# Performance work log

Hardware: AMD Instinct MI355X
Metric: run time of the kernel (lower is better)

## Reference

```python
import jax, jax.numpy as jnp
import numpy as np

# Dimensions
N, C_IN, C_OUT, T, V = 64, 64, 64, 256, 25   # batch, channels, frames, joints
K, G = 3, 8                                   # num_subset, groups


def batch_norm(x, gamma, beta, eps=1e-5):
    # BatchNorm2d in training mode: biased batch stats over (N, T, V) per channel.
    mean = jnp.mean(x, axis=(0, 2, 3), keepdims=True)
    var = jnp.var(x, axis=(0, 2, 3), keepdims=True)
    g = gamma.reshape(1, -1, 1, 1)
    b = beta.reshape(1, -1, 1, 1)
    return g * (x - mean) * jax.lax.rsqrt(var + eps) + b


def setup_inputs() -> dict:
    key = jax.random.key(0)
    k0, k1, k2 = jax.random.split(key, 3)
    x0 = jax.random.normal(k0, (N, C_IN, T, V), dtype=jnp.float32)
    # decoupled adjacency parameter [num_subset, groups, V, V] (non-negative, adjacency-like)
    decoupled_A = jax.random.uniform(k1, (K, G, V, V), dtype=jnp.float32)
    scale = float(np.sqrt(0.5 / (C_OUT * K)))
    linear_weight = jax.random.normal(k2, (C_IN, C_OUT * K), dtype=jnp.float32) * scale
    linear_bias = jnp.full((1, C_OUT * K, 1, 1), 1e-6, dtype=jnp.float32)
    bn0_gamma = jnp.ones((C_OUT * K,), dtype=jnp.float32)
    bn0_beta = jnp.zeros((C_OUT * K,), dtype=jnp.float32)
    bn_gamma = jnp.ones((C_OUT,), dtype=jnp.float32)
    bn_beta = jnp.zeros((C_OUT,), dtype=jnp.float32)
    return {
        "x0": x0,
        "decoupled_A": decoupled_A,
        "linear_weight": linear_weight,
        "linear_bias": linear_bias,
        "bn0_gamma": bn0_gamma,
        "bn0_beta": bn0_beta,
        "bn_gamma": bn_gamma,
        "bn_beta": bn_beta,
    }


def reference(x0, decoupled_A, linear_weight, linear_bias,
              bn0_gamma, bn0_beta, bn_gamma, bn_beta):
    # Expand grouped adjacency to per-output-channel: [K, C_OUT, V, V]
    learn_adj = jnp.tile(decoupled_A, (1, C_OUT // G, 1, 1))
    # Degree normalization: A @ diag(1/(colsum+1e-3)) == divide columns by column sums.
    deg = jnp.sum(learn_adj, axis=2, keepdims=True)          # [K, C_OUT, 1, V]
    normed_adj = learn_adj / (deg + 0.001)                    # [K, C_OUT, V, V]

    # Pointwise channel mix: [N, C_IN, T, V] -> [N, K*C_OUT, T, V]
    x = jnp.einsum('nctw,cd->ndtw', x0, linear_weight) + linear_bias
    x = batch_norm(x, bn0_gamma, bn0_beta)

    n, kc, t, v = x.shape
    x = x.reshape(n, K, kc // K, t, v)                        # [N, K, C_OUT, T, V]
    # Per-channel graph propagation summed over subsets.
    x = jnp.einsum('nkctv,kcvw->nctw', x, normed_adj)         # [N, C_OUT, T, V]
    x = batch_norm(x, bn_gamma, bn_beta)

    x = x + x0  # identity residual (in_channels == out_channels)
    return jax.nn.relu(x)
```

## Files before the change

### kernel.cpp

```cpp
#include <hip/hip_runtime.h>
#include <hip/hip_bf16.h>

#define N_    64
#define CIN   64
#define COUT  64
#define T_    256
#define V_    25
#define K_    3
#define G_    8
#define D_    192
#define TV    6400
#define P_    409600.0f
#define NBLK1 1600

typedef __attribute__((ext_vector_type(8))) short bf16x8;
typedef __attribute__((ext_vector_type(4))) float f32x4;

__device__ __forceinline__ float bf2f(unsigned short u) {
    unsigned int x = ((unsigned int)u) << 16;
    return __uint_as_float(x);
}
__device__ __forceinline__ unsigned short f2bf(float f) {
    unsigned int x = __float_as_uint(f);
    unsigned int lsb = (x >> 16) & 1u;
    x += 0x7fffu + lsb;
    return (unsigned short)(x >> 16);
}

__global__ __launch_bounds__(256, 4) void k1_mfma(const float* __restrict__ x0,
                                                  const float* __restrict__ W,
                                                  const float* __restrict__ bias,
                                                  unsigned short* __restrict__ z,
                                                  float* __restrict__ part) {
    __shared__ unsigned short zb[4][16 * 68];
    __shared__ float ps[4][12][16], pq[4][12][16];
    int p0  = blockIdx.x * 256;
    int n   = p0 / TV;
    int tvb = p0 % TV;
    int wv  = threadIdx.x >> 6;
    int l   = threadIdx.x & 63;
    int l15 = l & 15;
    int kg  = l >> 4;
    int wbase = tvb + wv * 64;
    const float* xn = x0 + (size_t)n * CIN * TV;

    bf16x8 afr[4][2];
#pragma unroll
    for (int m = 0; m < 4; ++m)
#pragma unroll
        for (int kk = 0; kk < 2; ++kk)
#pragma unroll
            for (int j = 0; j < 8; ++j) {
                int c = kk * 32 + kg * 8 + j;
                afr[m][kk][j] = (short)f2bf(xn[(size_t)c * TV + wbase + m * 16 + l15]);
            }

    unsigned short* zn = z + (size_t)n * D_ * TV;
    unsigned short* zw = &zb[wv][0];
#pragma unroll 1
    for (int dt = 0; dt < 12; ++dt) {
        int dcol = dt * 16 + l15;
        bf16x8 bfr[2];
#pragma unroll
        for (int kk = 0; kk < 2; ++kk)
#pragma unroll
            for (int j = 0; j < 8; ++j) {
                int c = kk * 32 + kg * 8 + j;
                bfr[kk][j] = (short)f2bf(W[c * D_ + dcol]);
            }
        float bv = bias[dcol];
        f32x4 acc[4];
#pragma unroll
        for (int m = 0; m < 4; ++m) {
            acc[m][0] = bv; acc[m][1] = bv; acc[m][2] = bv; acc[m][3] = bv;
        }
#pragma unroll
        for (int m = 0; m < 4; ++m) {
            acc[m] = __builtin_amdgcn_mfma_f32_16x16x32_bf16(afr[m][0], bfr[0], acc[m], 0, 0, 0);
            acc[m] = __builtin_amdgcn_mfma_f32_16x16x32_bf16(afr[m][1], bfr[1], acc[m], 0, 0, 0);
        }
        float s = 0.f, sq = 0.f;
#pragma unroll
        for (int m = 0; m < 4; ++m)
#pragma unroll
            for (int r = 0; r < 4; ++r) {
                float v = acc[m][r];
                s += v; sq += v * v;
            }
        s  += __shfl_xor(s, 16, 64);  s  += __shfl_xor(s, 32, 64);
        sq += __shfl_xor(sq, 16, 64); sq += __shfl_xor(sq, 32, 64);
        if (kg == 0) { ps[wv][dt][l15] = s; pq[wv][dt][l15] = sq; }
#pragma unroll
        for (int m = 0; m < 4; ++m) {
            uint2 pk;
            pk.x = (unsigned int)f2bf(acc[m][0]) | ((unsigned int)f2bf(acc[m][1]) << 16);
            pk.y = (unsigned int)f2bf(acc[m][2]) | ((unsigned int)f2bf(acc[m][3]) << 16);
            *(uint2*)(&zw[l15 * 68 + m * 16 + kg * 4]) = pk;
        }
#pragma unroll
        for (int i = 0; i < 4; ++i) {
            int dR  = i * 4 + kg;
            int tvo = l15 * 4;
            uint2 v = *(const uint2*)(&zw[dR * 68 + tvo]);
            *(uint2*)(zn + (size_t)(dt * 16 + dR) * TV + wbase + tvo) = v;
        }
    }
    __syncthreads();
    int tid = threadIdx.x;
    if (tid < D_) {
        int dt = tid >> 4, lo = tid & 15;
        float s = ps[0][dt][lo] + ps[1][dt][lo] + ps[2][dt][lo] + ps[3][dt][lo];
        float q = pq[0][dt][lo] + pq[1][dt][lo] + pq[2][dt][lo] + pq[3][dt][lo];
        part[(size_t)blockIdx.x * 384 + tid]        = s;
        part[(size_t)blockIdx.x * 384 + 192 + tid]  = q;
    }
}

__global__ __launch_bounds__(64) void k1c_reduce(const float* __restrict__ part,
                                                 float* __restrict__ sum0,
                                                 float* __restrict__ sumsq0) {
    int idx = blockIdx.x;
    int l = threadIdx.x;
    float s = 0.f;
    for (int b = l; b < NBLK1; b += 64) s += part[(size_t)b * 384 + idx];
#pragma unroll
    for (int off = 32; off > 0; off >>= 1) s += __shfl_down(s, off, 64);
    if (l == 0) {
        if (idx < D_) sum0[idx] = s;
        else          sumsq0[idx - D_] = s;
    }
}

__global__ __launch_bounds__(256, 1) void k2_prep(const float* __restrict__ A,
                                                  const float* __restrict__ g0,
                                                  const float* __restrict__ b0,
                                                  const float* __restrict__ sum0,
                                                  const float* __restrict__ sumsq0,
                                                  float* a, float* b,
                                                  float* nadj, float* bconst) {
    int tid = threadIdx.x;
    if (tid < D_) {
        float m   = sum0[tid] / P_;
        float var = sumsq0[tid] / P_ - m * m;
        float sc  = g0[tid] * rsqrtf(var + 1e-5f);
        a[tid] = sc;
        b[tid] = b0[tid] - sc * m;
    }
    for (int idx = tid; idx < K_ * G_ * V_; idx += 256) {
        int w  = idx % V_;
        int kg = idx / V_;
        const float* Ap = A + kg * V_ * V_;
        float cs = 0.f;
        for (int v = 0; v < V_; ++v) cs += Ap[v * V_ + w];
        float inv = 1.f / (cs + 1e-3f);
        for (int v = 0; v < V_; ++v) nadj[kg * V_ * V_ + v * V_ + w] = Ap[v * V_ + w] * inv;
    }
    __syncthreads();
    for (int idx = tid; idx < COUT * V_; idx += 256) {
        int c = idx / V_, w = idx % V_, g = c & 7;
        float s = 0.f;
        for (int k = 0; k < K_; ++k) {
            float bk = b[k * COUT + c];
            const float* np_ = nadj + (k * G_ + g) * V_ * V_;
            float cs = 0.f;
            for (int v = 0; v < V_; ++v) cs += np_[v * V_ + w];
            s += bk * cs;
        }
        bconst[idx] = s;
    }
}

__global__ __launch_bounds__(256, 2) void k3_adj(const unsigned short* __restrict__ z,
                                                 const float* __restrict__ a,
                                                 const float* __restrict__ nadj,
                                                 const float* __restrict__ bconst,
                                                 unsigned short* __restrict__ x2,
                                                 float* __restrict__ sum2,
                                                 float* __restrict__ sumsq2) {
    __shared__ float s_nadj[K_][625];
    __shared__ __align__(16) unsigned short zs[4][TV];
    int tid = threadIdx.x;
    int g   = blockIdx.x & 7;
    int pq  = blockIdx.x >> 3;
    int wv  = tid >> 6;
    int l   = tid & 63;
    int p   = pq * 4 + wv;
    int n   = p >> 3;
    int c   = (p & 7) * 8 + g;
    for (int idx = tid; idx < K_ * 625; idx += 256) {
        int k = idx / 625, r = idx % 625;
        s_nadj[k][r] = nadj[(k * 8 + g) * 625 + r];
    }
    __syncthreads();

    float acc[4][25];
#pragma unroll
    for (int w = 0; w < 25; ++w) {
        float bc = bconst[c * 25 + w];
#pragma unroll
        for (int j = 0; j < 4; ++j) acc[j][w] = bc;
    }

    uint4* zs4 = (uint4*)&zs[wv][0];
#pragma unroll 1
    for (int k = 0; k < K_; ++k) {
        int d = k * 64 + c;
        const uint4* row4 = (const uint4*)(z + ((size_t)n * D_ + d) * TV);
        for (int e = l; e < 800; e += 64) zs4[e] = row4[e];
        float ad = a[d];
#pragma unroll 1
        for (int v = 0; v < 25; ++v) {
            float za0 = ad * bf2f(zs[wv][(l      ) * 25 + v]);
            float za1 = ad * bf2f(zs[wv][(l +  64) * 25 + v]);
            float za2 = ad * bf2f(zs[wv][(l + 128) * 25 + v]);
            float za3 = ad * bf2f(zs[wv][(l + 192) * 25 + v]);
            const float* nr = &s_nadj[k][v * 25];
#pragma unroll
            for (int w = 0; w < 25; ++w) {
                float nv = nr[w];
                acc[0][w] = fmaf(za0, nv, acc[0][w]);
                acc[1][w] = fmaf(za1, nv, acc[1][w]);
                acc[2][w] = fmaf(za2, nv, acc[2][w]);
                acc[3][w] = fmaf(za3, nv, acc[3][w]);
            }
        }
    }

    unsigned short* xp = x2 + ((size_t)n * COUT + c) * TV;
    float s = 0.f, sq = 0.f;
#pragma unroll
    for (int j = 0; j < 4; ++j) {
        int t = l + 64 * j;
#pragma unroll
        for (int w = 0; w < 25; ++w) {
            float val = acc[j][w];
            s += val; sq += val * val;
            xp[t * 25 + w] = f2bf(val);
        }
    }
#pragma unroll
    for (int off = 32; off > 0; off >>= 1) {
        s  += __shfl_down(s,  off, 64);
        sq += __shfl_down(sq, off, 64);
    }
    if (l == 0) {
        atomicAdd(&sum2[c], s);
        atomicAdd(&sumsq2[c], sq);
    }
}

__global__ __launch_bounds__(256) void k4_final(const unsigned short* __restrict__ x2,
                                                const float* __restrict__ x0,
                                                const float* __restrict__ g2,
                                                const float* __restrict__ b2,
                                                const float* __restrict__ sum2,
                                                const float* __restrict__ sumsq2,
                                                float* __restrict__ out) {
    const int total4 = N_ * COUT * TV / 4;
    for (int i = blockIdx.x * 256 + threadIdx.x; i < total4; i += gridDim.x * 256) {
        int c = ((i * 4) / TV) & 63;
        float m   = sum2[c] * (1.f / P_);
        float var = sumsq2[c] * (1.f / P_) - m * m;
        float sc  = g2[c] * rsqrtf(var + 1e-5f);
        float sh  = b2[c] - sc * m;
        ushort4 u = ((const ushort4*)x2)[i];
        float4  x = ((const float4*)x0)[i];
        float4 o;
        o.x = fmaxf(sc * bf2f(u.x) + sh + x.x, 0.f);
        o.y = fmaxf(sc * bf2f(u.y) + sh + x.y, 0.f);
        o.z = fmaxf(sc * bf2f(u.z) + sh + x.z, 0.f);
        o.w = fmaxf(sc * bf2f(u.w) + sh + x.w, 0.f);
        ((float4*)out)[i] = o;
    }
}

extern "C" void kernel_launch(void* const* d_in, const int* in_sizes, int n_in,
                              void* d_out, int out_size, void* d_ws, size_t ws_size,
                              hipStream_t stream) {
    const float* x0   = (const float*)d_in[0];
    const float* A    = (const float*)d_in[1];
    const float* W    = (const float*)d_in[2];
    const float* bias = (const float*)d_in[3];
    const float* g0   = (const float*)d_in[4];
    const float* b0   = (const float*)d_in[5];
    const float* g2   = (const float*)d_in[6];
    const float* b2   = (const float*)d_in[7];

    char* ws = (char*)d_ws;
    unsigned short* z  = (unsigned short*)ws;
    unsigned short* x2 = (unsigned short*)(ws + 157286400ull);
    float* part = (float*)x2;
    float* fregion = (float*)(ws + 209715200ull);
    float* sum0   = fregion;
    float* sumsq0 = fregion + 192;
    float* sum2   = fregion + 384;
    float* sumsq2 = fregion + 448;
    float* a      = fregion + 512;
    float* b      = a + 192;
    float* nadj   = b + 192;
    float* bconst = nadj + 15000;

    hipMemsetAsync(fregion, 0, 512 * sizeof(float), stream);
    k1_mfma<<<NBLK1, 256, 0, stream>>>(x0, W, bias, z, part);
    k1c_reduce<<<384, 64, 0, stream>>>(part, sum0, sumsq0);
    k2_prep<<<1, 256, 0, stream>>>(A, g0, b0, sum0, sumsq0, a, b, nadj, bconst);
    k3_adj<<<1024, 256, 0, stream>>>(z, a, nadj, bconst, x2, sum2, sumsq2);
    k4_final<<<2048, 256, 0, stream>>>(x2, x0, g2, b2, sum2, sumsq2,
                                       (float*)d_out);
}
```

Before: 395.9 us.

## Move graph-propagation kernel to MFMA and split linear kernel by output half

The adjacency propagation kernel now computes each (n,c) row with bf16 MFMA tiles (t x v times v x w, zero-padded from 25 to 32) instead of scalar FMAs, using a smaller per-wave LDS buffer and four times as many blocks. It also stages the output through LDS so global stores are coalesced. The linear kernel splits the 192 output channels into two halves per block, preloads all of its weight fragments, and uses hardware packed bf16 conversion. Padding wastes some MFMA work, and rounding the scaled adjacency to bf16 adds precision loss.

```diff
diff --git a/kernel.cpp b/kernel.cpp
--- a/kernel.cpp
+++ b/kernel.cpp
@@ -11,7 +11,6 @@
 #define D_    192
 #define TV    6400
 #define P_    409600.0f
-#define NBLK1 1600
 
 typedef __attribute__((ext_vector_type(8))) short bf16x8;
 typedef __attribute__((ext_vector_type(4))) float f32x4;
@@ -26,22 +25,30 @@
     x += 0x7fffu + lsb;
     return (unsigned short)(x >> 16);
 }
-
-__global__ __launch_bounds__(256, 4) void k1_mfma(const float* __restrict__ x0,
+__device__ __forceinline__ unsigned int cvtpk(float lo, float hi) {
+    unsigned int r;
+    asm("v_cvt_pk_bf16_f32 %0, %1, %2" : "=v"(r) : "v"(lo), "v"(hi));
+    return r;
+}
+
+__global__ __launch_bounds__(256, 3) void k1_mfma(const float* __restrict__ x0,
                                                   const float* __restrict__ W,
                                                   const float* __restrict__ bias,
                                                   unsigned short* __restrict__ z,
                                                   float* __restrict__ part) {
     __shared__ unsigned short zb[4][16 * 68];
-    __shared__ float ps[4][12][16], pq[4][12][16];
-    int p0  = blockIdx.x * 256;
-    int n   = p0 / TV;
-    int tvb = p0 % TV;
-    int wv  = threadIdx.x >> 6;
-    int l   = threadIdx.x & 63;
-    int l15 = l & 15;
-    int kg  = l >> 4;
-    int wbase = tvb + wv * 64;
+    __shared__ float ps[4][6][16], pq[4][6][16];
+    int dh   = blockIdx.x & 1;
+    int rest = blockIdx.x >> 1;
+    int n    = rest / 25;
+    int tvb  = rest % 25;
+    int tid  = threadIdx.x;
+    int wv   = tid >> 6;
+    int l    = tid & 63;
+    int l15  = l & 15;
+    int kg   = l >> 4;
+    int wbase = tvb * 256 + wv * 64;
+    int d0    = dh * 96;
     const float* xn = x0 + (size_t)n * CIN * TV;
 
     bf16x8 afr[4][2];
@@ -50,25 +57,32 @@
 #pragma unroll
         for (int kk = 0; kk < 2; ++kk)
 #pragma unroll
-            for (int j = 0; j < 8; ++j) {
-                int c = kk * 32 + kg * 8 + j;
-                afr[m][kk][j] = (short)f2bf(xn[(size_t)c * TV + wbase + m * 16 + l15]);
+            for (int h = 0; h < 4; ++h) {
+                int c0 = kk * 32 + kg * 8 + 2 * h;
+                float f0 = xn[(size_t)c0 * TV + wbase + m * 16 + l15];
+                float f1 = xn[(size_t)(c0 + 1) * TV + wbase + m * 16 + l15];
+                ((unsigned int*)&afr[m][kk])[h] = cvtpk(f0, f1);
+            }
+
+    bf16x8 wfr[6][2];
+#pragma unroll
+    for (int dt = 0; dt < 6; ++dt)
+#pragma unroll
+        for (int kk = 0; kk < 2; ++kk)
+#pragma unroll
+            for (int h = 0; h < 4; ++h) {
+                int c0 = kk * 32 + kg * 8 + 2 * h;
+                int dcol = d0 + dt * 16 + l15;
+                float f0 = W[c0 * D_ + dcol];
+                float f1 = W[(c0 + 1) * D_ + dcol];
+                ((unsigned int*)&wfr[dt][kk])[h] = cvtpk(f0, f1);
             }
 
     unsigned short* zn = z + (size_t)n * D_ * TV;
     unsigned short* zw = &zb[wv][0];
-#pragma unroll 1
-    for (int dt = 0; dt < 12; ++dt) {
-        int dcol = dt * 16 + l15;
-        bf16x8 bfr[2];
-#pragma unroll
-        for (int kk = 0; kk < 2; ++kk)
-#pragma unroll
-            for (int j = 0; j < 8; ++j) {
-                int c = kk * 32 + kg * 8 + j;
-                bfr[kk][j] = (short)f2bf(W[c * D_ + dcol]);
-            }
-        float bv = bias[dcol];
+#pragma unroll
+    for (int dt = 0; dt < 6; ++dt) {
+        float bv = bias[d0 + dt * 16 + l15];
         f32x4 acc[4];
 #pragma unroll
         for (int m = 0; m < 4; ++m) {
@@ -76,25 +90,22 @@
         }
 #pragma unroll
         for (int m = 0; m < 4; ++m) {
-            acc[m] = __builtin_amdgcn_mfma_f32_16x16x32_bf16(afr[m][0], bfr[0], acc[m], 0, 0, 0);
-            acc[m] = __builtin_amdgcn_mfma_f32_16x16x32_bf16(afr[m][1], bfr[1], acc[m], 0, 0, 0);
+            acc[m] = __builtin_amdgcn_mfma_f32_16x16x32_bf16(afr[m][0], wfr[dt][0], acc[m], 0, 0, 0);
+            acc[m] = __builtin_amdgcn_mfma_f32_16x16x32_bf16(afr[m][1], wfr[dt][1], acc[m], 0, 0, 0);
         }
         float s = 0.f, sq = 0.f;
 #pragma unroll
         for (int m = 0; m < 4; ++m)
 #pragma unroll
-            for (int r = 0; r < 4; ++r) {
-                float v = acc[m][r];
-                s += v; sq += v * v;
-            }
+            for (int r = 0; r < 4; ++r) { float v = acc[m][r]; s += v; sq += v * v; }
         s  += __shfl_xor(s, 16, 64);  s  += __shfl_xor(s, 32, 64);
         sq += __shfl_xor(sq, 16, 64); sq += __shfl_xor(sq, 32, 64);
         if (kg == 0) { ps[wv][dt][l15] = s; pq[wv][dt][l15] = sq; }
 #pragma unroll
         for (int m = 0; m < 4; ++m) {
             uint2 pk;
-            pk.x = (unsigned int)f2bf(acc[m][0]) | ((unsigned int)f2bf(acc[m][1]) << 16);
-            pk.y = (unsigned int)f2bf(acc[m][2]) | ((unsigned int)f2bf(acc[m][3]) << 16);
+            pk.x = cvtpk(acc[m][0], acc[m][1]);
+            pk.y = cvtpk(acc[m][2], acc[m][3]);
             *(uint2*)(&zw[l15 * 68 + m * 16 + kg * 4]) = pk;
         }
 #pragma unroll
@@ -102,17 +113,16 @@
             int dR  = i * 4 + kg;
             int tvo = l15 * 4;
             uint2 v = *(const uint2*)(&zw[dR * 68 + tvo]);
-            *(uint2*)(zn + (size_t)(dt * 16 + dR) * TV + wbase + tvo) = v;
+            *(uint2*)(zn + (size_t)(d0 + dt * 16 + dR) * TV + wbase + tvo) = v;
         }
     }
     __syncthreads();
-    int tid = threadIdx.x;
-    if (tid < D_) {
+    if (tid < 96) {
         int dt = tid >> 4, lo = tid & 15;
         float s = ps[0][dt][lo] + ps[1][dt][lo] + ps[2][dt][lo] + ps[3][dt][lo];
         float q = pq[0][dt][lo] + pq[1][dt][lo] + pq[2][dt][lo] + pq[3][dt][lo];
-        part[(size_t)blockIdx.x * 384 + tid]        = s;
-        part[(size_t)blockIdx.x * 384 + 192 + tid]  = q;
+        part[(size_t)blockIdx.x * 192 + tid]      = s;
+        part[(size_t)blockIdx.x * 192 + 96 + tid] = q;
     }
 }
 
@@ -120,14 +130,17 @@
                                                  float* __restrict__ sum0,
                                                  float* __restrict__ sumsq0) {
     int idx = blockIdx.x;
+    int isq = idx >= 192;
+    int d   = idx - 192 * isq;
+    int dhh = d / 96, dl = d % 96;
     int l = threadIdx.x;
     float s = 0.f;
-    for (int b = l; b < NBLK1; b += 64) s += part[(size_t)b * 384 + idx];
+    for (int tb = l; tb < 1600; tb += 64)
+        s += part[(size_t)(tb * 2 + dhh) * 192 + isq * 96 + dl];
 #pragma unroll
     for (int off = 32; off > 0; off >>= 1) s += __shfl_down(s, off, 64);
     if (l == 0) {
-        if (idx < D_) sum0[idx] = s;
-        else          sumsq0[idx - D_] = s;
+        if (isq) sumsq0[d] = s; else sum0[d] = s;
     }
 }
 
@@ -170,73 +183,93 @@
     }
 }
 
-__global__ __launch_bounds__(256, 2) void k3_adj(const unsigned short* __restrict__ z,
+__global__ __launch_bounds__(256, 4) void k3_adj(const unsigned short* __restrict__ z,
                                                  const float* __restrict__ a,
                                                  const float* __restrict__ nadj,
                                                  const float* __restrict__ bconst,
                                                  unsigned short* __restrict__ x2,
                                                  float* __restrict__ sum2,
                                                  float* __restrict__ sumsq2) {
-    __shared__ float s_nadj[K_][625];
-    __shared__ __align__(16) unsigned short zs[4][TV];
-    int tid = threadIdx.x;
-    int g   = blockIdx.x & 7;
-    int pq  = blockIdx.x >> 3;
-    int wv  = tid >> 6;
-    int l   = tid & 63;
-    int p   = pq * 4 + wv;
-    int n   = p >> 3;
-    int c   = (p & 7) * 8 + g;
-    for (int idx = tid; idx < K_ * 625; idx += 256) {
-        int k = idx / 625, r = idx % 625;
-        s_nadj[k][r] = nadj[(k * 8 + g) * 625 + r];
-    }
-    __syncthreads();
-
-    float acc[4][25];
-#pragma unroll
-    for (int w = 0; w < 25; ++w) {
-        float bc = bconst[c * 25 + w];
-#pragma unroll
-        for (int j = 0; j < 4; ++j) acc[j][w] = bc;
-    }
-
-    uint4* zs4 = (uint4*)&zs[wv][0];
+    __shared__ __align__(16) unsigned short buf[4][1600];
+    int n = blockIdx.x >> 6;
+    int c = blockIdx.x & 63;
+    int g = c & 7;
+    int tid = threadIdx.x, wv = tid >> 6, l = tid & 63;
+    int l15 = l & 15, kg = l >> 4;
+
+    f32x4 acc[4][2];
+#pragma unroll
+    for (int wt = 0; wt < 2; ++wt) {
+        int w = wt * 16 + l15;
+        float bc = (w < 25) ? bconst[c * 25 + w] : 0.f;
+#pragma unroll
+        for (int tt = 0; tt < 4; ++tt) {
+            acc[tt][wt][0] = bc; acc[tt][wt][1] = bc;
+            acc[tt][wt][2] = bc; acc[tt][wt][3] = bc;
+        }
+    }
+
+    unsigned short* bw = &buf[wv][0];
 #pragma unroll 1
     for (int k = 0; k < K_; ++k) {
         int d = k * 64 + c;
-        const uint4* row4 = (const uint4*)(z + ((size_t)n * D_ + d) * TV);
-        for (int e = l; e < 800; e += 64) zs4[e] = row4[e];
+        const uint4* src = (const uint4*)(z + ((size_t)n * D_ + d) * TV + wv * 1600);
+        uint4* dst4 = (uint4*)bw;
+        for (int e = l; e < 200; e += 64) dst4[e] = src[e];
         float ad = a[d];
-#pragma unroll 1
-        for (int v = 0; v < 25; ++v) {
-            float za0 = ad * bf2f(zs[wv][(l      ) * 25 + v]);
-            float za1 = ad * bf2f(zs[wv][(l +  64) * 25 + v]);
-            float za2 = ad * bf2f(zs[wv][(l + 128) * 25 + v]);
-            float za3 = ad * bf2f(zs[wv][(l + 192) * 25 + v]);
-            const float* nr = &s_nadj[k][v * 25];
-#pragma unroll
-            for (int w = 0; w < 25; ++w) {
-                float nv = nr[w];
-                acc[0][w] = fmaf(za0, nv, acc[0][w]);
-                acc[1][w] = fmaf(za1, nv, acc[1][w]);
-                acc[2][w] = fmaf(za2, nv, acc[2][w]);
-                acc[3][w] = fmaf(za3, nv, acc[3][w]);
-            }
-        }
-    }
-
-    unsigned short* xp = x2 + ((size_t)n * COUT + c) * TV;
+        const float* nb = nadj + (k * 8 + g) * 625;
+        bf16x8 bfr[2];
+#pragma unroll
+        for (int wt = 0; wt < 2; ++wt) {
+            int w = wt * 16 + l15;
+            int wc = (w < 25) ? w : 0;
+#pragma unroll
+            for (int h = 0; h < 4; ++h) {
+                int v0 = kg * 8 + 2 * h;
+                float f0 = (v0     < 25) ? ad * nb[v0 * 25 + wc]       : 0.f;
+                float f1 = (v0 + 1 < 25) ? ad * nb[(v0 + 1) * 25 + wc] : 0.f;
+                ((unsigned int*)&bfr[wt])[h] = cvtpk(f0, f1);
+            }
+        }
+#pragma unroll
+        for (int tt = 0; tt < 4; ++tt) {
+            int tl = tt * 16 + l15;
+            bf16x8 af;
+#pragma unroll
+            for (int h = 0; h < 4; ++h) {
+                int v0 = kg * 8 + 2 * h;
+                unsigned int lo = (v0     < 25) ? (unsigned int)bw[tl * 25 + v0]     : 0u;
+                unsigned int hi = (v0 + 1 < 25) ? (unsigned int)bw[tl * 25 + v0 + 1] : 0u;
+                ((unsigned int*)&af)[h] = lo | (hi << 16);
+            }
+            acc[tt][0] = __builtin_amdgcn_mfma_f32_16x16x32_bf16(af, bfr[0], acc[tt][0], 0, 0, 0);
+            acc[tt][1] = __builtin_amdgcn_mfma_f32_16x16x32_bf16(af, bfr[1], acc[tt][1], 0, 0, 0);
+        }
+    }
+#pragma unroll
+    for (int tt = 0; tt < 4; ++tt)
+#pragma unroll
+        for (int wt = 0; wt < 2; ++wt) {
+            int w = wt * 16 + l15;
+            if (w < 25) {
+#pragma unroll
+                for (int r = 0; r < 4; ++r) {
+                    int tl = tt * 16 + kg * 4 + r;
+                    bw[tl * 25 + w] = f2bf(acc[tt][wt][r]);
+                }
+            }
+        }
     float s = 0.f, sq = 0.f;
-#pragma unroll
-    for (int j = 0; j < 4; ++j) {
-        int t = l + 64 * j;
-#pragma unroll
-        for (int w = 0; w < 25; ++w) {
-            float val = acc[j][w];
-            s += val; sq += val * val;
-            xp[t * 25 + w] = f2bf(val);
-        }
+    unsigned short* xb = x2 + ((size_t)n * COUT + c) * TV + wv * 1600;
+    for (int e = l; e < 200; e += 64) {
+        uint4 vv = ((const uint4*)bw)[e];
+        const unsigned short* u = (const unsigned short*)&vv;
+#pragma unroll
+        for (int i = 0; i < 8; ++i) {
+            float f = bf2f(u[i]);
+            s += f; sq += f * f;
+        }
+        ((uint4*)xb)[e] = vv;
     }
 #pragma unroll
     for (int off = 32; off > 0; off >>= 1) {
@@ -301,10 +334,10 @@
     float* bconst = nadj + 15000;
 
     hipMemsetAsync(fregion, 0, 512 * sizeof(float), stream);
-    k1_mfma<<<NBLK1, 256, 0, stream>>>(x0, W, bias, z, part);
+    k1_mfma<<<3200, 256, 0, stream>>>(x0, W, bias, z, part);
     k1c_reduce<<<384, 64, 0, stream>>>(part, sum0, sumsq0);
     k2_prep<<<1, 256, 0, stream>>>(A, g0, b0, sum0, sumsq0, a, b, nadj, bconst);
-    k3_adj<<<1024, 256, 0, stream>>>(z, a, nadj, bconst, x2, sum2, sumsq2);
+    k3_adj<<<4096, 256, 0, stream>>>(z, a, nadj, bconst, x2, sum2, sumsq2);
     k4_final<<<2048, 256, 0, stream>>>(x2, x0, g2, b2, sum2, sumsq2,
                                        (float*)d_out);
 }
```

Result: slower. 439.8 us (+11.1%).
